# Kernel tuning notes

Hardware: AMD Instinct MI355X
Metric: run time of the kernel (lower is better)

Reference implementation:

```python
import jax, jax.numpy as jnp
import numpy as np

IN_DIM = 128
HIDDEN = 128


def setup_inputs() -> dict:
    key = jax.random.key(0)
    k1, k2, k3, k4, k5 = jax.random.split(key, 5)
    bound_ih = 1.0 / np.sqrt(IN_DIM)
    bound_hh = 1.0 / np.sqrt(HIDDEN)
    return {
        "x": jax.random.normal(k1, (256, 2048, IN_DIM), dtype=jnp.float32),
        "W_ih": jax.random.uniform(k2, (HIDDEN, IN_DIM), minval=-bound_ih, maxval=bound_ih, dtype=jnp.float32),
        "b_ih": jax.random.uniform(k3, (HIDDEN,), minval=-bound_ih, maxval=bound_ih, dtype=jnp.float32),
        "W_hh": jax.random.uniform(k4, (HIDDEN, HIDDEN), minval=-bound_hh, maxval=bound_hh, dtype=jnp.float32),
        "b_hh": jax.random.uniform(k5, (HIDDEN,), minval=-bound_hh, maxval=bound_hh, dtype=jnp.float32),
    }


def reference(x, W_ih, b_ih, W_hh, b_hh):
    B, S, _ = x.shape
    # Precompute input projection for all timesteps in one big GEMM: [B,S,H]
    xw = jnp.einsum("bsi,hi->bsh", x, W_ih) + b_ih
    h0 = jnp.zeros((B, W_hh.shape[0]), dtype=x.dtype)

    def step(h, xw_t):
        h_new = jnp.tanh(xw_t + h @ W_hh.T + b_hh)
        return h_new, None

    # scan over time axis: move S to leading dim
    h_final, _ = jax.lax.scan(step, h0, jnp.swapaxes(xw, 0, 1))
    return h_final
```

## Files before the change

kernel.cpp:

```cpp
#include <hip/hip_runtime.h>


#define BATCH 256
#define SEQ   2048
#define HID   128
#define CH    16
#define NCHUNK (SEQ / CH)

typedef __attribute__((ext_vector_type(8))) short bf16x8;
typedef __attribute__((ext_vector_type(4))) float f32x4;
typedef __attribute__((ext_vector_type(2))) float f32x2;

template <int CTRL>
__device__ __forceinline__ float dpp_movf(float x) {
    return __int_as_float(__builtin_amdgcn_mov_dpp(__float_as_int(x), CTRL, 0xF, 0xF, true));
}

__device__ __forceinline__ float tanh_fast(float x) {
    x = fminf(fmaxf(x, -12.0f), 12.0f);
    float e = __expf(2.0f * x);
    return 1.0f - __fdividef(2.0f, e + 1.0f);
}

__device__ __forceinline__ void bf16_split(float v, short& hi, short& lo) {
    unsigned u = __float_as_uint(v);
    unsigned hb = (u + 0x8000u) & 0xFFFF0000u;
    float hf = __uint_as_float(hb);
    float r = v - hf;
    unsigned ru = __float_as_uint(r);
    hi = (short)(hb >> 16);
    lo = (short)((ru + 0x8000u) >> 16);
}

__global__ __launch_bounds__(512, 2) void rnn_scan_kernel(
    const float* __restrict__ x,
    const float* __restrict__ Wih,
    const float* __restrict__ bih,
    const float* __restrict__ Whh,
    const float* __restrict__ bhh,
    float* __restrict__ out)
{
    const int b = blockIdx.x;
    const int t = threadIdx.x;
    const int g = t >> 4;
    const int c = t & 15;
    const int colbase = c << 3;
    const int rowbase = g << 2;
    const int lane = t & 63;
    const int w = t >> 6;

    __shared__ __align__(16) ushort xbf[2][2][CH * HID];
    __shared__ __align__(16) float  xwbuf[2][CH * HID];
    __shared__ __align__(16) float  hbuf[2][192];

    f32x2 wh[4][4];
#pragma unroll
    for (int r = 0; r < 4; ++r) {
        const float* ph = Whh + (rowbase + r) * HID + colbase;
        float4 u0 = *(const float4*)(ph);
        float4 u1 = *(const float4*)(ph + 4);
        wh[r][0] = f32x2{u0.x, u0.y};
        wh[r][1] = f32x2{u0.z, u0.w};
        wh[r][2] = f32x2{u1.x, u1.y};
        wh[r][3] = f32x2{u1.z, u1.w};
    }

    const int bcol = (w << 4) + (lane & 15);
    const float biasv = bih[bcol] + bhh[bcol];
    bf16x8 bhi[4], blo[4];
#pragma unroll
    for (int kk = 0; kk < 4; ++kk) {
        const float* src = Wih + bcol * HID + kk * 32 + ((lane >> 4) << 3);
        float4 u0 = *(const float4*)(src);
        float4 u1 = *(const float4*)(src + 4);
        short hh, ll;
        bf16_split(u0.x, hh, ll); bhi[kk][0] = hh; blo[kk][0] = ll;
        bf16_split(u0.y, hh, ll); bhi[kk][1] = hh; blo[kk][1] = ll;
        bf16_split(u0.z, hh, ll); bhi[kk][2] = hh; blo[kk][2] = ll;
        bf16_split(u0.w, hh, ll); bhi[kk][3] = hh; blo[kk][3] = ll;
        bf16_split(u1.x, hh, ll); bhi[kk][4] = hh; blo[kk][4] = ll;
        bf16_split(u1.y, hh, ll); bhi[kk][5] = hh; blo[kk][5] = ll;
        bf16_split(u1.z, hh, ll); bhi[kk][6] = hh; blo[kk][6] = ll;
        bf16_split(u1.w, hh, ll); bhi[kk][7] = hh; blo[kk][7] = ll;
    }

    const int m = c & 3;
    const int o = ((m & 1) << 1) | ((m >> 1) & 1);
    const int row0 = rowbase + o;
    const int hw = row0 + ((row0 >> 3) << 2);

    const float* xsrc = x + (size_t)b * (SEQ * HID);

    auto stage_bf16 = [&](float4 q, int buf) {
        const int srow = t >> 5;
        const int sw = ((srow << 8) + ((t & 31) << 3)) ^ ((srow & 7) << 4);
        short h0, l0, h1, l1, h2, l2, h3, l3;
        bf16_split(q.x, h0, l0); bf16_split(q.y, h1, l1);
        bf16_split(q.z, h2, l2); bf16_split(q.w, h3, l3);
        uint2 ph, pl;
        ph.x = (unsigned)(ushort)h0 | ((unsigned)(ushort)h1 << 16);
        ph.y = (unsigned)(ushort)h2 | ((unsigned)(ushort)h3 << 16);
        pl.x = (unsigned)(ushort)l0 | ((unsigned)(ushort)l1 << 16);
        pl.y = (unsigned)(ushort)l2 | ((unsigned)(ushort)l3 << 16);
        *(uint2*)((char*)&xbf[buf][0][0] + sw) = ph;
        *(uint2*)((char*)&xbf[buf][1][0] + sw) = pl;
    };

    auto compute_xw = [&](int mm) {
        const int buf = mm & 1;
        const int arow = lane & 15;
        const int rowb = (arow << 8) + ((lane >> 4) << 4);
        const int swz = (arow & 7) << 4;
        const char* hp = (const char*)&xbf[buf][0][0];
        const char* lp = (const char*)&xbf[buf][1][0];
        f32x4 acc0 = {0.0f, 0.0f, 0.0f, 0.0f};
        f32x4 acc1 = {0.0f, 0.0f, 0.0f, 0.0f};
#pragma unroll
        for (int kk = 0; kk < 4; ++kk) {
            const int off = (rowb + kk * 64) ^ swz;
            bf16x8 ah = *(const bf16x8*)(hp + off);
            bf16x8 al = *(const bf16x8*)(lp + off);
            f32x4& acc = (kk & 1) ? acc1 : acc0;
            acc = __builtin_amdgcn_mfma_f32_16x16x32_bf16(ah, bhi[kk], acc, 0, 0, 0);
            acc = __builtin_amdgcn_mfma_f32_16x16x32_bf16(ah, blo[kk], acc, 0, 0, 0);
            acc = __builtin_amdgcn_mfma_f32_16x16x32_bf16(al, bhi[kk], acc, 0, 0, 0);
        }
        float* xw = &xwbuf[buf][0];
        const int crow = (lane >> 4) << 2;
#pragma unroll
        for (int r = 0; r < 4; ++r)
            xw[(crow + r) * HID + bcol] = acc0[r] + acc1[r] + biasv;
    };

    {
        const float4* gp = (const float4*)xsrc;
        float4 a0 = gp[t];
        float4 a1 = gp[512 + t];
        stage_bf16(a0, 0);
        stage_bf16(a1, 1);
    }
    if (t < 192) hbuf[0][t] = 0.0f;
    __syncthreads();
    compute_xw(0);
    __syncthreads();

    for (int n = 0; n < NCHUNK; ++n) {
        float4 q0;
        const bool pf = (n + 2 < NCHUNK);
        if (pf) {
            const float4* gp = (const float4*)(xsrc + (size_t)(n + 2) * (CH * HID));
            q0 = gp[t];
        }
        const float* xwc = &xwbuf[n & 1][0] + row0;
        const float* h0p = &hbuf[0][12 * c];
        const float* h1p = &hbuf[1][12 * c];
#pragma unroll
        for (int s = 0; s < CH; ++s) {
            float xwv = xwc[s * HID];
            const float* hr = (s & 1) ? h1p : h0p;
            float4 hv0 = *(const float4*)(hr);
            float4 hv1 = *(const float4*)(hr + 4);
            f32x2 hp0 = {hv0.x, hv0.y};
            f32x2 hp1 = {hv0.z, hv0.w};
            f32x2 hp2 = {hv1.x, hv1.y};
            f32x2 hp3 = {hv1.z, hv1.w};

            float a[4];
#pragma unroll
            for (int r = 0; r < 4; ++r) {
                f32x2 acc = wh[r][0] * hp0;
                acc = __builtin_elementwise_fma(wh[r][1], hp1, acc);
                acc = __builtin_elementwise_fma(wh[r][2], hp2, acc);
                acc = __builtin_elementwise_fma(wh[r][3], hp3, acc);
                a[r] = acc.x + acc.y;
            }

            const bool b0 = (c & 1) != 0;
            const bool b1 = (c & 2) != 0;
            float k0 = b0 ? a[2] : a[0], s0 = b0 ? a[0] : a[2];
            float k1 = b0 ? a[3] : a[1], s1 = b0 ? a[1] : a[3];
            float t0 = k0 + dpp_movf<0xB1>(s0);
            float t1 = k1 + dpp_movf<0xB1>(s1);
            float k2 = b1 ? t1 : t0, s2 = b1 ? t0 : t1;
            float u = k2 + dpp_movf<0x4E>(s2);
            u += dpp_movf<0x124>(u);
            u += dpp_movf<0x128>(u);

            float hval = tanh_fast(u + xwv);
            if (c < 4) {
                hbuf[(s & 1) ^ 1][hw] = hval;
            }

            if (s == 0 && n + 1 < NCHUNK) compute_xw(n + 1);
            if (s == CH - 1 && pf) stage_bf16(q0, n & 1);

            __syncthreads();
        }
    }
    if (t < HID) out[(size_t)b * HID + t] = hbuf[0][t + ((t >> 3) << 2)];
}

extern "C" void kernel_launch(void* const* d_in, const int* in_sizes, int n_in,
                              void* d_out, int out_size, void* d_ws, size_t ws_size,
                              hipStream_t stream) {
    const float* x   = (const float*)d_in[0];
    const float* Wih = (const float*)d_in[1];
    const float* bih = (const float*)d_in[2];
    const float* Whh = (const float*)d_in[3];
    const float* bhh = (const float*)d_in[4];
    float* out = (float*)d_out;

    rnn_scan_kernel<<<BATCH, 512, 0, stream>>>(x, Wih, bih, Whh, bhh, out);
}
```

Before: 1.113 ms.

## Process two batch rows per block to interleave independent recurrences

Each block now handles two batch elements, with separate shared buffers per sequence and interleaved mat-vec, reductions and tanh for both chains. The grid shrinks to half the blocks and launch bounds drop to one block per CU. The goal is to hide the serial latency of each step and halve the number of per-step barriers per batch row by giving each thread two independent dependency chains. The cost is more registers and shared memory per block, and fewer blocks than CUs (128 blocks on 256 CUs), which leaves half the device idle.

Result: slower. 1.463 ms (+31.4%).

```diff
diff --git a/kernel.cpp b/kernel.cpp
--- a/kernel.cpp
+++ b/kernel.cpp
@@ -32,7 +32,7 @@
     lo = (short)((ru + 0x8000u) >> 16);
 }
 
-__global__ __launch_bounds__(512, 2) void rnn_scan_kernel(
+__global__ __launch_bounds__(512, 1) void rnn_scan_kernel(
     const float* __restrict__ x,
     const float* __restrict__ Wih,
     const float* __restrict__ bih,
@@ -40,7 +40,7 @@
     const float* __restrict__ bhh,
     float* __restrict__ out)
 {
-    const int b = blockIdx.x;
+    const int b0 = blockIdx.x << 1;
     const int t = threadIdx.x;
     const int g = t >> 4;
     const int c = t & 15;
@@ -49,9 +49,9 @@
     const int lane = t & 63;
     const int w = t >> 6;
 
-    __shared__ __align__(16) ushort xbf[2][2][CH * HID];
-    __shared__ __align__(16) float  xwbuf[2][CH * HID];
-    __shared__ __align__(16) float  hbuf[2][192];
+    __shared__ __align__(16) ushort xbf[2][2][2][CH * HID];
+    __shared__ __align__(16) float  xwbuf[2][2][CH * HID];
+    __shared__ __align__(16) float  hbuf[2][2][192];
 
     f32x2 wh[4][4];
 #pragma unroll
@@ -89,9 +89,10 @@
     const int row0 = rowbase + o;
     const int hw = row0 + ((row0 >> 3) << 2);
 
-    const float* xsrc = x + (size_t)b * (SEQ * HID);
-
-    auto stage_bf16 = [&](float4 q, int buf) {
+    const float* xsA = x + (size_t)b0 * (SEQ * HID);
+    const float* xsB = xsA + (size_t)(SEQ * HID);
+
+    auto stage_bf16 = [&](float4 q, int bi, int buf) {
         const int srow = t >> 5;
         const int sw = ((srow << 8) + ((t & 31) << 3)) ^ ((srow & 7) << 4);
         short h0, l0, h1, l1, h2, l2, h3, l3;
@@ -102,17 +103,17 @@
         ph.y = (unsigned)(ushort)h2 | ((unsigned)(ushort)h3 << 16);
         pl.x = (unsigned)(ushort)l0 | ((unsigned)(ushort)l1 << 16);
         pl.y = (unsigned)(ushort)l2 | ((unsigned)(ushort)l3 << 16);
-        *(uint2*)((char*)&xbf[buf][0][0] + sw) = ph;
-        *(uint2*)((char*)&xbf[buf][1][0] + sw) = pl;
+        *(uint2*)((char*)&xbf[bi][buf][0][0] + sw) = ph;
+        *(uint2*)((char*)&xbf[bi][buf][1][0] + sw) = pl;
     };
 
-    auto compute_xw = [&](int mm) {
+    auto compute_xw = [&](int bi, int mm) {
         const int buf = mm & 1;
         const int arow = lane & 15;
         const int rowb = (arow << 8) + ((lane >> 4) << 4);
         const int swz = (arow & 7) << 4;
-        const char* hp = (const char*)&xbf[buf][0][0];
-        const char* lp = (const char*)&xbf[buf][1][0];
+        const char* hp = (const char*)&xbf[bi][buf][0][0];
+        const char* lp = (const char*)&xbf[bi][buf][1][0];
         f32x4 acc0 = {0.0f, 0.0f, 0.0f, 0.0f};
         f32x4 acc1 = {0.0f, 0.0f, 0.0f, 0.0f};
 #pragma unroll
@@ -125,7 +126,7 @@
             acc = __builtin_amdgcn_mfma_f32_16x16x32_bf16(ah, blo[kk], acc, 0, 0, 0);
             acc = __builtin_amdgcn_mfma_f32_16x16x32_bf16(al, bhi[kk], acc, 0, 0, 0);
         }
-        float* xw = &xwbuf[buf][0];
+        float* xw = &xwbuf[bi][buf][0];
         const int crow = (lane >> 4) << 2;
 #pragma unroll
         for (int r = 0; r < 4; ++r)
@@ -133,71 +134,103 @@
     };
 
     {
-        const float4* gp = (const float4*)xsrc;
-        float4 a0 = gp[t];
-        float4 a1 = gp[512 + t];
-        stage_bf16(a0, 0);
-        stage_bf16(a1, 1);
-    }
-    if (t < 192) hbuf[0][t] = 0.0f;
+        const float4* gpA = (const float4*)xsA;
+        const float4* gpB = (const float4*)xsB;
+        float4 a0 = gpA[t], a1 = gpA[512 + t];
+        float4 c0 = gpB[t], c1 = gpB[512 + t];
+        stage_bf16(a0, 0, 0); stage_bf16(a1, 0, 1);
+        stage_bf16(c0, 1, 0); stage_bf16(c1, 1, 1);
+    }
+    if (t < 192) { hbuf[0][0][t] = 0.0f; hbuf[1][0][t] = 0.0f; }
     __syncthreads();
-    compute_xw(0);
+    compute_xw(0, 0);
+    compute_xw(1, 0);
     __syncthreads();
 
     for (int n = 0; n < NCHUNK; ++n) {
-        float4 q0;
+        float4 qA, qB;
         const bool pf = (n + 2 < NCHUNK);
         if (pf) {
-            const float4* gp = (const float4*)(xsrc + (size_t)(n + 2) * (CH * HID));
-            q0 = gp[t];
+            const size_t off = (size_t)(n + 2) * (CH * HID);
+            qA = ((const float4*)(xsA + off))[t];
+            qB = ((const float4*)(xsB + off))[t];
         }
-        const float* xwc = &xwbuf[n & 1][0] + row0;
-        const float* h0p = &hbuf[0][12 * c];
-        const float* h1p = &hbuf[1][12 * c];
+        const float* xwcA = &xwbuf[0][n & 1][0] + row0;
+        const float* xwcB = &xwbuf[1][n & 1][0] + row0;
+        const float* hA0 = &hbuf[0][0][12 * c];
+        const float* hA1 = &hbuf[0][1][12 * c];
+        const float* hB0 = &hbuf[1][0][12 * c];
+        const float* hB1 = &hbuf[1][1][12 * c];
 #pragma unroll
         for (int s = 0; s < CH; ++s) {
-            float xwv = xwc[s * HID];
-            const float* hr = (s & 1) ? h1p : h0p;
-            float4 hv0 = *(const float4*)(hr);
-            float4 hv1 = *(const float4*)(hr + 4);
-            f32x2 hp0 = {hv0.x, hv0.y};
-            f32x2 hp1 = {hv0.z, hv0.w};
-            f32x2 hp2 = {hv1.x, hv1.y};
-            f32x2 hp3 = {hv1.z, hv1.w};
-
-            float a[4];
+            const float* hrA = (s & 1) ? hA1 : hA0;
+            const float* hrB = (s & 1) ? hB1 : hB0;
+            float4 hvA0 = *(const float4*)(hrA);
+            float4 hvA1 = *(const float4*)(hrA + 4);
+            float4 hvB0 = *(const float4*)(hrB);
+            float4 hvB1 = *(const float4*)(hrB + 4);
+            float xwvA = xwcA[s * HID];
+            float xwvB = xwcB[s * HID];
+
+            f32x2 pA0 = {hvA0.x, hvA0.y}, pA1 = {hvA0.z, hvA0.w};
+            f32x2 pA2 = {hvA1.x, hvA1.y}, pA3 = {hvA1.z, hvA1.w};
+            f32x2 pB0 = {hvB0.x, hvB0.y}, pB1 = {hvB0.z, hvB0.w};
+            f32x2 pB2 = {hvB1.x, hvB1.y}, pB3 = {hvB1.z, hvB1.w};
+
+            float aA[4], aB[4];
 #pragma unroll
             for (int r = 0; r < 4; ++r) {
-                f32x2 acc = wh[r][0] * hp0;
-                acc = __builtin_elementwise_fma(wh[r][1], hp1, acc);
-                acc = __builtin_elementwise_fma(wh[r][2], hp2, acc);
-                acc = __builtin_elementwise_fma(wh[r][3], hp3, acc);
-                a[r] = acc.x + acc.y;
+                f32x2 acc = wh[r][0] * pA0;
+                acc = __builtin_elementwise_fma(wh[r][1], pA1, acc);
+                acc = __builtin_elementwise_fma(wh[r][2], pA2, acc);
+                acc = __builtin_elementwise_fma(wh[r][3], pA3, acc);
+                aA[r] = acc.x + acc.y;
+                f32x2 bcc = wh[r][0] * pB0;
+                bcc = __builtin_elementwise_fma(wh[r][1], pB1, bcc);
+                bcc = __builtin_elementwise_fma(wh[r][2], pB2, bcc);
+                bcc = __builtin_elementwise_fma(wh[r][3], pB3, bcc);
+                aB[r] = bcc.x + bcc.y;
             }
 
-            const bool b0 = (c & 1) != 0;
-            const bool b1 = (c & 2) != 0;
-            float k0 = b0 ? a[2] : a[0], s0 = b0 ? a[0] : a[2];
-            float k1 = b0 ? a[3] : a[1], s1 = b0 ? a[1] : a[3];
-            float t0 = k0 + dpp_movf<0xB1>(s0);
-            float t1 = k1 + dpp_movf<0xB1>(s1);
-            float k2 = b1 ? t1 : t0, s2 = b1 ? t0 : t1;
-            float u = k2 + dpp_movf<0x4E>(s2);
-            u += dpp_movf<0x124>(u);
-            u += dpp_movf<0x128>(u);
-
-            float hval = tanh_fast(u + xwv);
+            const bool q0 = (c & 1) != 0;
+            const bool q1 = (c & 2) != 0;
+            float kA0 = q0 ? aA[2] : aA[0], sA0 = q0 ? aA[0] : aA[2];
+            float kA1 = q0 ? aA[3] : aA[1], sA1 = q0 ? aA[1] : aA[3];
+            float kB0 = q0 ? aB[2] : aB[0], sB0 = q0 ? aB[0] : aB[2];
+            float kB1 = q0 ? aB[3] : aB[1], sB1 = q0 ? aB[1] : aB[3];
+            float tA0 = kA0 + dpp_movf<0xB1>(sA0);
+            float tA1 = kA1 + dpp_movf<0xB1>(sA1);
+            float tB0 = kB0 + dpp_movf<0xB1>(sB0);
+            float tB1 = kB1 + dpp_movf<0xB1>(sB1);
+            float kA2 = q1 ? tA1 : tA0, sA2 = q1 ? tA0 : tA1;
+            float kB2 = q1 ? tB1 : tB0, sB2 = q1 ? tB0 : tB1;
+            float uA = kA2 + dpp_movf<0x4E>(sA2);
+            float uB = kB2 + dpp_movf<0x4E>(sB2);
+            uA += dpp_movf<0x124>(uA);
+            uB += dpp_movf<0x124>(uB);
+            uA += dpp_movf<0x128>(uA);
+            uB += dpp_movf<0x128>(uB);
+
+            float hA = tanh_fast(uA + xwvA);
+            float hB = tanh_fast(uB + xwvB);
             if (c < 4) {
-                hbuf[(s & 1) ^ 1][hw] = hval;
+                hbuf[0][(s & 1) ^ 1][hw] = hA;
+                hbuf[1][(s & 1) ^ 1][hw] = hB;
             }
 
-            if (s == 0 && n + 1 < NCHUNK) compute_xw(n + 1);
-            if (s == CH - 1 && pf) stage_bf16(q0, n & 1);
+            if (s == 0 && n + 1 < NCHUNK) compute_xw(0, n + 1);
+            if (s == 1 && n + 1 < NCHUNK) compute_xw(1, n + 1);
+            if (s == 14 && pf) stage_bf16(qA, 0, n & 1);
+            if (s == 15 && pf) stage_bf16(qB, 1, n & 1);
 
             __syncthreads();
         }
     }
-    if (t < HID) out[(size_t)b * HID + t] = hbuf[0][t + ((t >> 3) << 2)];
+    if (t < HID) {
+        const int pi = t + ((t >> 3) << 2);
+        out[(size_t)b0 * HID + t] = hbuf[0][0][pi];
+        out[(size_t)(b0 + 1) * HID + t] = hbuf[1][0][pi];
+    }
 }
 
 extern "C" void kernel_launch(void* const* d_in, const int* in_sizes, int n_in,
@@ -210,5 +243,5 @@
     const float* bhh = (const float*)d_in[4];
     float* out = (float*)d_out;
 
-    rnn_scan_kernel<<<BATCH, 512, 0, stream>>>(x, Wih, bih, Whh, bhh, out);
-}
+    rnn_scan_kernel<<<BATCH / 2, 512, 0, stream>>>(x, Wih, bih, Whh, bhh, out);
+}
```
